# Kernel tuning notes

Measured on AMD Instinct MI355X. Metric: run time of the kernel, lower is better.

Reference implementation:

```python
import jax, jax.numpy as jnp
import numpy as np


def log_g(x):
    # log of g(x) = where(x>=0, x+0.5, sigmoid(x))
    return jnp.where(x >= 0, jnp.log(jax.nn.relu(x) + 0.5), -jax.nn.softplus(-x))


def mingru_layer(x, h0, w, b):
    # x: (B,S,In), h0: (B,1,H), w: (2H,In), b: (2H,)
    B, S, _ = x.shape
    gh = jnp.einsum('bsi,oi->bso', x, w) + b          # (B,S,2H)
    H = gh.shape[-1] // 2
    gate, hidden = gh[..., :H], gh[..., H:]
    log_z = -jax.nn.softplus(-gate)                    # log sigmoid(gate)
    log_coeffs = -jax.nn.softplus(gate)                # log(1 - z)
    log_tilde_h = log_g(hidden)
    log_values = jnp.concatenate([jnp.log(h0), log_z + log_tilde_h], axis=1)  # (B,S+1,H)
    a_star = jnp.concatenate(
        [jnp.zeros((B, 1, H), dtype=x.dtype), jnp.cumsum(log_coeffs, axis=1)], axis=1
    )                                                  # (B,S+1,H)
    log_h = a_star + jax.lax.cumlogsumexp(log_values - a_star, axis=1)
    return jnp.exp(log_h)[:, 1:]                       # (B,S,H)


def setup_inputs() -> dict:
    key = jax.random.key(0)
    k = jax.random.split(key, 5)
    B, S, D, H = 8, 4096, 512, 512
    sc = 1.0 / np.sqrt(D)
    return {
        'x': jax.random.normal(k[0], (B, S, D), jnp.float32),
        'w0': jax.random.normal(k[1], (2 * H, D), jnp.float32) * sc,
        'b0': jax.random.normal(k[2], (2 * H,), jnp.float32) * 0.01,
        'w1': jax.random.normal(k[3], (2 * H, H), jnp.float32) * sc,
        'b1': jax.random.normal(k[4], (2 * H,), jnp.float32) * 0.01,
    }


def reference(x, w0, b0, w1, b1):
    B = x.shape[0]
    # init_hidden_state: g(zeros) = 0.5
    next_hidden = []
    inp = x
    for (w, b) in ((w0, b0), (w1, b1)):
        H = w.shape[0] // 2
        h0 = jnp.full((B, 1, H), 0.5, dtype=x.dtype)
        out = mingru_layer(inp, h0, w, b)
        next_hidden.append(out[:, -1:])
        inp = out
    return (out, jnp.stack(next_hidden))  # (B,S,H), (L,B,1,H)
```

## Files before the change

kernel.cpp:

```cpp
#include <hip/hip_runtime.h>
#include <math.h>


typedef unsigned short u16;
typedef __attribute__((ext_vector_type(8))) short short8;
typedef __attribute__((ext_vector_type(4))) float f32x4;

__device__ __forceinline__ u16 f2bf(float f) {
    unsigned int u = __float_as_uint(f);
    return (u16)((u + 0x7fffu + ((u >> 16) & 1u)) >> 16);
}
__device__ __forceinline__ float bf2f(u16 u) {
    return __uint_as_float(((unsigned int)u) << 16);
}
__device__ __forceinline__ void async16(const void* g, void* l) {
    __builtin_amdgcn_global_load_lds(
        (const __attribute__((address_space(1))) unsigned int*)g,
        (__attribute__((address_space(3))) unsigned int*)l, 16, 0, 0);
}
__device__ __forceinline__ float fastrcp(float x) { return __builtin_amdgcn_rcpf(x); }

__device__ __forceinline__ void coeff_val(float gate, float hid, float& c, float& v)
{
    float cc = fastrcp(1.0f + __expf(gate));
    float gp = hid + 0.5f;
    float gn = fastrcp(1.0f + __expf(-hid));
    float g  = (hid >= 0.0f) ? gp : gn;
    c = cc;
    v = (1.0f - cc) * g;
}

__global__ __launch_bounds__(256) void cast3(
    const float* __restrict__ x,  u16* __restrict__ xb,  int nx4,
    const float* __restrict__ w0, u16* __restrict__ w0b,
    const float* __restrict__ w1, u16* __restrict__ w1b, int nw4)
{
    int i = blockIdx.x * 256 + threadIdx.x;
    const float* src; u16* dst; int idx;
    if (i < nx4)                { src = x;  dst = xb;  idx = i; }
    else if (i < nx4 + nw4)     { src = w0; dst = w0b; idx = i - nx4; }
    else if (i < nx4 + 2 * nw4) { src = w1; dst = w1b; idx = i - nx4 - nw4; }
    else return;
    float4 v = ((const float4*)src)[idx];
    ushort4 o = make_ushort4(f2bf(v.x), f2bf(v.y), f2bf(v.z), f2bf(v.w));
    ((ushort4*)dst)[idx] = o;
}

#define TST 136

__global__ __launch_bounds__(256) void gemm_fused(
    const u16* __restrict__ A, const u16* __restrict__ W,
    const float* __restrict__ bias, u16* __restrict__ gh,
    float* __restrict__ cA, float* __restrict__ cV, int K)
{
    __shared__ __align__(16) u16 lds[128 * TST];

    const int tid  = threadIdx.x;
    const int d    = blockIdx.y * 8 + blockIdx.x;
    const int cpx  = (int)(gridDim.x * gridDim.y) >> 3;
    const int t0   = (d & 7) * cpx + (d >> 3);
    const int bn   = t0 & 7;
    const int bm   = t0 >> 3;
    const int lane = tid & 63;
    const int wave = tid >> 6;
    const int wm   = (wave >> 1) * 64;
    const int wn   = (wave & 1) * 64;
    const int w1   = wave & 1;
    const int fm   = lane & 15;
    const int kb   = lane >> 4;

    const int r0 = tid >> 2, q0 = (tid & 3) ^ (r0 & 3);
    const int r1 = r0 + 64,  q1 = (tid & 3) ^ (r1 & 3);
    const u16* Ap0 = A + (size_t)(bm * 128 + r0) * 512 + q0 * 8;
    const u16* Ap1 = A + (size_t)(bm * 128 + r1) * 512 + q1 * 8;
    const int wr0 = bn * 64 + (r0 & 31) + ((r0 & 32) ? 512 : 0);
    const int wr1 = bn * 64 + (r1 & 31) + 32 + ((r1 & 32) ? 512 : 0);
    const u16* Wp0 = W + (size_t)wr0 * 512 + q0 * 8;
    const u16* Wp1 = W + (size_t)wr1 * 512 + q1 * 8;

    int offA[4], offB[4];
    #pragma unroll
    for (int i = 0; i < 4; ++i) {
        const int rowA = wm + i * 16 + fm;
        offA[i] = rowA * 64 + ((kb ^ (rowA & 3)) * 16);
        const int rowB = wn + i * 16 + fm;
        offB[i] = rowB * 64 + ((kb ^ (rowB & 3)) * 16);
    }

    f32x4 acc[4][4];
    #pragma unroll
    for (int i = 0; i < 4; ++i)
        #pragma unroll
        for (int j = 0; j < 4; ++j)
            acc[i][j] = (f32x4){0.f, 0.f, 0.f, 0.f};

    const char* AsB = (const char*)lds;

#define STAGE(NB) do { \
    char* dst_ = (char*)lds + (NB); \
    async16(Ap0, dst_ + tid * 16); \
    async16(Ap1, dst_ + (tid + 256) * 16); \
    async16(Wp0, dst_ + 8192 + tid * 16); \
    async16(Wp1, dst_ + 8192 + (tid + 256) * 16); \
    Ap0 += 32; Ap1 += 32; Wp0 += 32; Wp1 += 32; } while (0)

#define COMPUTE(CB) do { \
    const char* src_ = AsB + (CB); \
    short8 av[4], bw[4]; \
    _Pragma("unroll") for (int i = 0; i < 4; ++i) \
        av[i] = *(const short8*)(src_ + offA[i]); \
    _Pragma("unroll") for (int j = 0; j < 4; ++j) \
        bw[j] = *(const short8*)(src_ + 8192 + offB[j]); \
    _Pragma("unroll") for (int i = 0; i < 4; ++i) \
        _Pragma("unroll") for (int j = 0; j < 4; ++j) \
            acc[i][j] = __builtin_amdgcn_mfma_f32_16x16x32_bf16( \
                av[i], bw[j], acc[i][j], 0, 0, 0); \
} while (0)

    int cb = 0;
    STAGE(0);
    __syncthreads();
    for (int kt = 32; kt < K; kt += 32) {
        STAGE(cb ^ 16384);
        COMPUTE(cb);
        __syncthreads();
        cb ^= 16384;
    }
    COMPUTE(cb);
    __syncthreads();

#undef STAGE
#undef COMPUTE

    float bg[2], bh[2];
    #pragma unroll
    for (int jj = 0; jj < 2; ++jj) {
        const int chl = w1 * 32 + jj * 16 + fm;
        bg[jj] = bias[bn * 64 + chl];
        bh[jj] = bias[512 + bn * 64 + chl];
    }
    unsigned int* ldsw = (unsigned int*)lds;
    #pragma unroll
    for (int i = 0; i < 4; ++i)
        #pragma unroll
        for (int jj = 0; jj < 2; ++jj) {
            const int chl = w1 * 32 + jj * 16 + fm;
            const f32x4 g4 = acc[i][jj];
            const f32x4 h4 = acc[i][jj + 2];
            #pragma unroll
            for (int r = 0; r < 4; ++r) {
                const int row = wm + i * 16 + kb * 4 + r;
                float c, v;
                coeff_val(g4[r] + bg[jj], h4[r] + bh[jj], c, v);
                ldsw[row * 68 + chl] = (unsigned int)f2bf(c)
                                     | ((unsigned int)f2bf(v) << 16);
            }
        }
    __syncthreads();

    #pragma unroll
    for (int it = 0; it < 8; ++it) {
        const int row = it * 16 + (tid >> 4);
        const int sc  = (tid & 15) * 8;
        short8 vv = *(const short8*)&lds[row * TST + sc];
        *(short8*)&gh[(size_t)(bm * 128 + row) * 1024 + bn * 128 + sc] = vv;
    }

    const int ch = tid & 63;
    const int ck = tid >> 6;
    float Aa = 1.f, Vv = 0.f;
    #pragma unroll 4
    for (int s = 0; s < 32; ++s) {
        const unsigned int p = ldsw[(ck * 32 + s) * 68 + ch];
        const float c = bf2f((u16)p);
        const float v = bf2f((u16)(p >> 16));
        Aa *= c;
        Vv = fmaf(c, Vv, v);
    }
    const int bb  = bm >> 5;
    const int ckg = (bm & 31) * 4 + ck;
    const size_t idx = ((size_t)(bb * 128 + ckg)) * 512 + bn * 64 + ch;
    cA[idx] = Aa;
    cV[idx] = Vv;
}

__global__ __launch_bounds__(256) void scan_pass2(
    const float* __restrict__ cA, const float* __restrict__ cV,
    float* __restrict__ carry, int Nc)
{
    const int tid = threadIdx.x;
    const int b = blockIdx.x;
    float s0 = 0.5f, s1 = 0.5f;
    #pragma unroll 8
    for (int ck = 0; ck < Nc; ++ck) {
        const size_t idx = (size_t)(b * Nc + ck) * 512 + 2 * tid;
        *(float2*)(carry + idx) = make_float2(s0, s1);
        float2 a = *(const float2*)(cA + idx);
        float2 v = *(const float2*)(cV + idx);
        s0 = fmaf(a.x, s0, v.x);
        s1 = fmaf(a.y, s1, v.y);
    }
}

template <bool OUT_BF16>
__global__ __launch_bounds__(256) void scan_pass3(
    const u16* __restrict__ gh, const float* __restrict__ carry,
    void* __restrict__ outv, float* __restrict__ nh,
    int S, int Lc, int Nc)
{
    const int tid = threadIdx.x;
    const int b  = blockIdx.x / Nc;
    const int ck = blockIdx.x % Nc;
    const u16* base = gh + (size_t)(b * S + ck * Lc) * 1024 + 4 * tid;
    const size_t cidx = (size_t)(b * Nc + ck) * 512 + 2 * tid;
    float2 st = *(const float2*)(carry + cidx);
    float h0 = st.x, h1 = st.y;
    const size_t obase = (size_t)(b * S + ck * Lc) * 512 + 2 * tid;
    #pragma unroll 4
    for (int s = 0; s < Lc; ++s) {
        ushort4 q = *(const ushort4*)(base + (size_t)s * 1024);
        h0 = fmaf(bf2f(q.x), h0, bf2f(q.y));
        h1 = fmaf(bf2f(q.z), h1, bf2f(q.w));
        if (OUT_BF16) {
            ushort2 o = make_ushort2(f2bf(h0), f2bf(h1));
            *(ushort2*)((u16*)outv + obase + (size_t)s * 512) = o;
        } else {
            *(float2*)((float*)outv + obase + (size_t)s * 512) = make_float2(h0, h1);
        }
    }
    if (ck == Nc - 1)
        *(float2*)(nh + (size_t)b * 512 + 2 * tid) = make_float2(h0, h1);
}

extern "C" void kernel_launch(void* const* d_in, const int* in_sizes, int n_in,
                              void* d_out, int out_size, void* d_ws, size_t ws_size,
                              hipStream_t stream)
{
    const float* x  = (const float*)d_in[0];
    const float* w0 = (const float*)d_in[1];
    const float* b0 = (const float*)d_in[2];
    const float* w1 = (const float*)d_in[3];
    const float* b1 = (const float*)d_in[4];
    float* out = (float*)d_out;

    const int B = 8, S = 4096, K = 512;
    const int M = B * S;
    const int Lc = 32, Nc = S / Lc;

    u16* gh  = (u16*)d_ws;
    u16* xb  = gh  + (size_t)M * 1024;
    u16* h0b = xb;
    u16* w0b = xb  + (size_t)M * 512;
    u16* w1b = w0b + (size_t)1024 * 512;
    float* cA    = (float*)(w1b + (size_t)1024 * 512);
    float* cV    = cA + (size_t)B * Nc * 512;
    float* carry = cV + (size_t)B * Nc * 512;

    float* nh0 = out + (size_t)M * 512;
    float* nh1 = nh0 + (size_t)B * 512;

    dim3 blk(256);
    dim3 ggrid(8, M / 128);
    dim3 sgrid(B * Nc);

    const int nx4 = M * K / 4;
    const int nw4 = 1024 * K / 4;
    cast3<<<dim3((nx4 + 2 * nw4 + 255) / 256), blk, 0, stream>>>(
        x, xb, nx4, w0, w0b, w1, w1b, nw4);

    gemm_fused<<<ggrid, blk, 0, stream>>>(xb, w0b, b0, gh, cA, cV, K);
    scan_pass2<<<dim3(B), blk, 0, stream>>>(cA, cV, carry, Nc);
    scan_pass3<true><<<sgrid, blk, 0, stream>>>(gh, carry, h0b, nh0, S, Lc, Nc);

    gemm_fused<<<ggrid, blk, 0, stream>>>(h0b, w1b, b1, gh, cA, cV, K);
    scan_pass2<<<dim3(B), blk, 0, stream>>>(cA, cV, carry, Nc);
    scan_pass3<false><<<sgrid, blk, 0, stream>>>(gh, carry, out, nh1, S, Lc, Nc);
}
```

Before: 288.2 us.

## Widen cast and scan accesses, change LDS swizzle, unroll fixed-K GEMM loop

The cast kernel now converts eight floats per thread and writes 16-byte bf16 stores. The scan pass3 uses 128 threads that each handle four channels, giving 16-byte gh loads and wider output stores. The GEMM LDS XOR swizzle now keys on (row>>1)&3 to change the bank-conflict pattern. The K loop is hard-coded for K=512 and unrolled into ping-pong stages with constant buffer offsets. The K generalisation is lost, and halving the scan's thread count per block may reduce latency hiding.

```diff
diff --git a/kernel.cpp b/kernel.cpp
--- a/kernel.cpp
+++ b/kernel.cpp
@@ -31,19 +31,24 @@
 }
 
 __global__ __launch_bounds__(256) void cast3(
-    const float* __restrict__ x,  u16* __restrict__ xb,  int nx4,
+    const float* __restrict__ x,  u16* __restrict__ xb,  int nx8,
     const float* __restrict__ w0, u16* __restrict__ w0b,
-    const float* __restrict__ w1, u16* __restrict__ w1b, int nw4)
+    const float* __restrict__ w1, u16* __restrict__ w1b, int nw8)
 {
     int i = blockIdx.x * 256 + threadIdx.x;
     const float* src; u16* dst; int idx;
-    if (i < nx4)                { src = x;  dst = xb;  idx = i; }
-    else if (i < nx4 + nw4)     { src = w0; dst = w0b; idx = i - nx4; }
-    else if (i < nx4 + 2 * nw4) { src = w1; dst = w1b; idx = i - nx4 - nw4; }
+    if (i < nx8)                { src = x;  dst = xb;  idx = i; }
+    else if (i < nx8 + nw8)     { src = w0; dst = w0b; idx = i - nx8; }
+    else if (i < nx8 + 2 * nw8) { src = w1; dst = w1b; idx = i - nx8 - nw8; }
     else return;
-    float4 v = ((const float4*)src)[idx];
-    ushort4 o = make_ushort4(f2bf(v.x), f2bf(v.y), f2bf(v.z), f2bf(v.w));
-    ((ushort4*)dst)[idx] = o;
+    const float4* s4 = (const float4*)src + 2 * (size_t)idx;
+    float4 a = s4[0], b = s4[1];
+    short8 o;
+    o[0] = (short)f2bf(a.x); o[1] = (short)f2bf(a.y);
+    o[2] = (short)f2bf(a.z); o[3] = (short)f2bf(a.w);
+    o[4] = (short)f2bf(b.x); o[5] = (short)f2bf(b.y);
+    o[6] = (short)f2bf(b.z); o[7] = (short)f2bf(b.w);
+    ((short8*)dst)[idx] = o;
 }
 
 #define TST 136
@@ -51,7 +56,7 @@
 __global__ __launch_bounds__(256) void gemm_fused(
     const u16* __restrict__ A, const u16* __restrict__ W,
     const float* __restrict__ bias, u16* __restrict__ gh,
-    float* __restrict__ cA, float* __restrict__ cV, int K)
+    float* __restrict__ cA, float* __restrict__ cV)
 {
     __shared__ __align__(16) u16 lds[128 * TST];
 
@@ -69,8 +74,8 @@
     const int fm   = lane & 15;
     const int kb   = lane >> 4;
 
-    const int r0 = tid >> 2, q0 = (tid & 3) ^ (r0 & 3);
-    const int r1 = r0 + 64,  q1 = (tid & 3) ^ (r1 & 3);
+    const int r0 = tid >> 2, q0 = (tid & 3) ^ ((r0 >> 1) & 3);
+    const int r1 = r0 + 64,  q1 = (tid & 3) ^ ((r1 >> 1) & 3);
     const u16* Ap0 = A + (size_t)(bm * 128 + r0) * 512 + q0 * 8;
     const u16* Ap1 = A + (size_t)(bm * 128 + r1) * 512 + q1 * 8;
     const int wr0 = bn * 64 + (r0 & 31) + ((r0 & 32) ? 512 : 0);
@@ -82,9 +87,9 @@
     #pragma unroll
     for (int i = 0; i < 4; ++i) {
         const int rowA = wm + i * 16 + fm;
-        offA[i] = rowA * 64 + ((kb ^ (rowA & 3)) * 16);
+        offA[i] = rowA * 64 + ((kb ^ ((rowA >> 1) & 3)) * 16);
         const int rowB = wn + i * 16 + fm;
-        offB[i] = rowB * 64 + ((kb ^ (rowB & 3)) * 16);
+        offB[i] = rowB * 64 + ((kb ^ ((rowB >> 1) & 3)) * 16);
     }
 
     f32x4 acc[4][4];
@@ -105,28 +110,26 @@
     Ap0 += 32; Ap1 += 32; Wp0 += 32; Wp1 += 32; } while (0)
 
 #define COMPUTE(CB) do { \
-    const char* src_ = AsB + (CB); \
     short8 av[4], bw[4]; \
     _Pragma("unroll") for (int i = 0; i < 4; ++i) \
-        av[i] = *(const short8*)(src_ + offA[i]); \
+        av[i] = *(const short8*)(AsB + offA[i] + (CB)); \
     _Pragma("unroll") for (int j = 0; j < 4; ++j) \
-        bw[j] = *(const short8*)(src_ + 8192 + offB[j]); \
+        bw[j] = *(const short8*)(AsB + 8192 + offB[j] + (CB)); \
     _Pragma("unroll") for (int i = 0; i < 4; ++i) \
         _Pragma("unroll") for (int j = 0; j < 4; ++j) \
             acc[i][j] = __builtin_amdgcn_mfma_f32_16x16x32_bf16( \
                 av[i], bw[j], acc[i][j], 0, 0, 0); \
 } while (0)
 
-    int cb = 0;
     STAGE(0);
     __syncthreads();
-    for (int kt = 32; kt < K; kt += 32) {
-        STAGE(cb ^ 16384);
-        COMPUTE(cb);
-        __syncthreads();
-        cb ^= 16384;
-    }
-    COMPUTE(cb);
+    #pragma unroll 1
+    for (int it = 0; it < 7; ++it) {
+        STAGE(16384); COMPUTE(0);     __syncthreads();
+        STAGE(0);     COMPUTE(16384); __syncthreads();
+    }
+    STAGE(16384); COMPUTE(0); __syncthreads();
+    COMPUTE(16384);
     __syncthreads();
 
 #undef STAGE
@@ -203,33 +206,36 @@
 }
 
 template <bool OUT_BF16>
-__global__ __launch_bounds__(256) void scan_pass3(
+__global__ __launch_bounds__(128) void scan_pass3(
     const u16* __restrict__ gh, const float* __restrict__ carry,
     void* __restrict__ outv, float* __restrict__ nh,
     int S, int Lc, int Nc)
 {
-    const int tid = threadIdx.x;
+    const int th = threadIdx.x;
     const int b  = blockIdx.x / Nc;
     const int ck = blockIdx.x % Nc;
-    const u16* base = gh + (size_t)(b * S + ck * Lc) * 1024 + 4 * tid;
-    const size_t cidx = (size_t)(b * Nc + ck) * 512 + 2 * tid;
-    float2 st = *(const float2*)(carry + cidx);
-    float h0 = st.x, h1 = st.y;
-    const size_t obase = (size_t)(b * S + ck * Lc) * 512 + 2 * tid;
-    #pragma unroll 4
+    const u16* base = gh + (size_t)(b * S + ck * Lc) * 1024 + 8 * th;
+    const size_t cidx = (size_t)(b * Nc + ck) * 512 + 4 * th;
+    float4 st = *(const float4*)(carry + cidx);
+    float h0 = st.x, h1 = st.y, h2 = st.z, h3 = st.w;
+    const size_t obase = (size_t)(b * S + ck * Lc) * 512 + 4 * th;
+    #pragma unroll 8
     for (int s = 0; s < Lc; ++s) {
-        ushort4 q = *(const ushort4*)(base + (size_t)s * 1024);
-        h0 = fmaf(bf2f(q.x), h0, bf2f(q.y));
-        h1 = fmaf(bf2f(q.z), h1, bf2f(q.w));
+        short8 q = *(const short8*)(base + (size_t)s * 1024);
+        h0 = fmaf(bf2f((u16)q[0]), h0, bf2f((u16)q[1]));
+        h1 = fmaf(bf2f((u16)q[2]), h1, bf2f((u16)q[3]));
+        h2 = fmaf(bf2f((u16)q[4]), h2, bf2f((u16)q[5]));
+        h3 = fmaf(bf2f((u16)q[6]), h3, bf2f((u16)q[7]));
         if (OUT_BF16) {
-            ushort2 o = make_ushort2(f2bf(h0), f2bf(h1));
-            *(ushort2*)((u16*)outv + obase + (size_t)s * 512) = o;
+            ushort4 o = make_ushort4(f2bf(h0), f2bf(h1), f2bf(h2), f2bf(h3));
+            *(ushort4*)((u16*)outv + obase + (size_t)s * 512) = o;
         } else {
-            *(float2*)((float*)outv + obase + (size_t)s * 512) = make_float2(h0, h1);
+            *(float4*)((float*)outv + obase + (size_t)s * 512)
+                = make_float4(h0, h1, h2, h3);
         }
     }
     if (ck == Nc - 1)
-        *(float2*)(nh + (size_t)b * 512 + 2 * tid) = make_float2(h0, h1);
+        *(float4*)(nh + (size_t)b * 512 + 4 * th) = make_float4(h0, h1, h2, h3);
 }
 
 extern "C" void kernel_launch(void* const* d_in, const int* in_sizes, int n_in,
@@ -263,16 +269,16 @@
     dim3 ggrid(8, M / 128);
     dim3 sgrid(B * Nc);
 
-    const int nx4 = M * K / 4;
-    const int nw4 = 1024 * K / 4;
-    cast3<<<dim3((nx4 + 2 * nw4 + 255) / 256), blk, 0, stream>>>(
-        x, xb, nx4, w0, w0b, w1, w1b, nw4);
-
-    gemm_fused<<<ggrid, blk, 0, stream>>>(xb, w0b, b0, gh, cA, cV, K);
+    const int nx8 = M * K / 8;
+    const int nw8 = 1024 * K / 8;
+    cast3<<<dim3((nx8 + 2 * nw8 + 255) / 256), blk, 0, stream>>>(
+        x, xb, nx8, w0, w0b, w1, w1b, nw8);
+
+    gemm_fused<<<ggrid, blk, 0, stream>>>(xb, w0b, b0, gh, cA, cV);
     scan_pass2<<<dim3(B), blk, 0, stream>>>(cA, cV, carry, Nc);
-    scan_pass3<true><<<sgrid, blk, 0, stream>>>(gh, carry, h0b, nh0, S, Lc, Nc);
-
-    gemm_fused<<<ggrid, blk, 0, stream>>>(h0b, w1b, b1, gh, cA, cV, K);
+    scan_pass3<true><<<sgrid, dim3(128), 0, stream>>>(gh, carry, h0b, nh0, S, Lc, Nc);
+
+    gemm_fused<<<ggrid, blk, 0, stream>>>(h0b, w1b, b1, gh, cA, cV);
     scan_pass2<<<dim3(B), blk, 0, stream>>>(cA, cV, carry, Nc);
-    scan_pass3<false><<<sgrid, blk, 0, stream>>>(gh, carry, out, nh1, S, Lc, Nc);
-}
+    scan_pass3<false><<<sgrid, dim3(128), 0, stream>>>(gh, carry, out, nh1, S, Lc, Nc);
+}
```

New measurement: 291.4 us. About the same (+1.1%).
